# Performance work log

Measured on AMD Instinct MI355X. Metric: run time of the kernel, lower is better.

Reference implementation:

```python
import jax, jax.numpy as jnp
import numpy as np

N, E, B = 100000, 1200000, 512
IN_DIM, HID, K, NCLS = 64, 64, 3, 10


def setup_inputs() -> dict:
    key = jax.random.key(0)
    ks = jax.random.split(key, 10)
    features = jax.random.normal(ks[0], (N, IN_DIM), jnp.float32)
    edge_src = jax.random.randint(ks[1], (E,), 0, N)
    edge_dst = jax.random.randint(ks[2], (E,), 0, N)
    graph_ids = jnp.sort(jax.random.randint(ks[3], (N,), 0, B))
    s1 = float(1.0 / np.sqrt(IN_DIM))
    W1 = jax.random.uniform(ks[4], (IN_DIM, HID), jnp.float32, -s1, s1)
    b1 = jnp.zeros((HID,), jnp.float32)
    s2 = float(1.0 / np.sqrt(HID))
    W2 = jax.random.uniform(ks[5], (HID, HID), jnp.float32, -s2, s2)
    b2 = jnp.zeros((HID,), jnp.float32)
    s3 = float(1.0 / np.sqrt(HID * 3))
    cw = jax.random.uniform(ks[6], (HID, HID, 3), jnp.float32, -s3, s3)
    cb = jax.random.uniform(ks[7], (HID,), jnp.float32, -s3, s3)
    Wc = jax.random.uniform(ks[8], (HID, NCLS), jnp.float32, -s2, s2)
    bc = jax.random.uniform(ks[9], (NCLS,), jnp.float32, -s2, s2)
    return dict(features=features, edge_src=edge_src, edge_dst=edge_dst,
                graph_ids=graph_ids, num_graphs=B,
                W1=W1, b1=b1, W2=W2, b2=b2, cw=cw, cb=cb, Wc=Wc, bc=bc)


def graph_conv(h, src, dst, W, b, n_nodes):
    # DGL GraphConv, norm='both', allow_zero_in_degree (degrees clamped to 1)
    ones = jnp.ones((src.shape[0],), h.dtype)
    out_deg = jnp.zeros((n_nodes,), h.dtype).at[src].add(ones)
    in_deg = jnp.zeros((n_nodes,), h.dtype).at[dst].add(ones)
    norm_s = jax.lax.rsqrt(jnp.clip(out_deg, 1.0, None))
    norm_d = jax.lax.rsqrt(jnp.clip(in_deg, 1.0, None))
    m = (h * norm_s[:, None]) @ W  # weight first; math identical to agg-first
    agg = jnp.zeros((n_nodes, W.shape[1]), h.dtype).at[dst].add(m[src])
    return agg * norm_d[:, None] + b


def sort_pool(h, gid, num_graphs, k):
    # DGL SortPooling: sort each node's features ascending along feature dim,
    # then take top-k nodes per graph by last feature value (descending),
    # zero-padding graphs with < k nodes. Output [num_graphs, k*D].
    hs = jnp.sort(h, axis=-1)
    key = hs[:, -1]
    order = jnp.lexsort((-key, gid))  # gid asc, key desc
    gid_s = gid[order]
    hs_s = hs[order]
    n = gid.shape[0]
    start = jnp.full((num_graphs,), n).at[gid_s].min(jnp.arange(n))
    rank = jnp.arange(n) - start[gid_s]  # within-graph rank by key desc
    mask = rank < k
    slot = gid_s * k + jnp.clip(rank, 0, k - 1)
    out = jnp.zeros((num_graphs * k, hs.shape[-1]), h.dtype).at[slot].add(
        jnp.where(mask[:, None], hs_s, jnp.zeros((), h.dtype)))
    return out.reshape(num_graphs, k * hs.shape[-1])


def reference(features, edge_src, edge_dst, graph_ids, num_graphs,
              W1, b1, W2, b2, cw, cb, Wc, bc):
    n = features.shape[0]
    h = jax.nn.relu(graph_conv(features, edge_src, edge_dst, W1, b1, n))
    h = jax.nn.relu(graph_conv(h, edge_src, edge_dst, W2, b2, n))
    p = sort_pool(h, graph_ids, num_graphs, K)          # [B, K*HID]
    x = p.reshape(num_graphs, HID, K)                    # faithful torch reshape
    # Conv1d(kernel=3, stride=1) on length-3 input -> length-1 output
    y = jax.nn.relu(jnp.einsum('bct,oct->bo', x, cw) + cb)
    return y @ Wc + bc
```

## Files before the change

kernel.cpp:

```cpp
#include <hip/hip_runtime.h>
#include <hip/hip_bf16.h>


#define PART_F 25088
#define QUART_F (PART_F / 4)
#define MCH  128
#define MCHS 32

__device__ __forceinline__ unsigned long long nib2b(unsigned int x) {
  unsigned long long lo = x & 0x0F0F0F0Fu;
  unsigned long long hi = (x >> 4) & 0x0F0F0F0Fu;
  lo = (lo | (lo << 16)) & 0x0000FFFF0000FFFFull;
  lo = (lo | (lo << 8))  & 0x00FF00FF00FF00FFull;
  hi = (hi | (hi << 16)) & 0x0000FFFF0000FFFFull;
  hi = (hi | (hi << 8))  & 0x00FF00FF00FF00FFull;
  return lo | (hi << 8);
}

__global__ void __launch_bounds__(256) k_histgemm(
    const int* __restrict__ esrc, const int* __restrict__ edst,
    unsigned char* __restrict__ hd4, unsigned char* __restrict__ hs4,
    const float* __restrict__ in, const float* __restrict__ W,
    float* __restrict__ mout, int N, int E, int NP, int histBlocks) {
  __shared__ float smem[12800];
  const int t = threadIdx.x;
  if (blockIdx.x < histBlocks) {
    unsigned int* lc = (unsigned int*)smem;
    const int b = blockIdx.x;
    const int a = (b < MCH) ? 0 : 1;
    const int m = a ? (b - MCH) : b;
    const int mch = a ? MCHS : MCH;
    const int* __restrict__ arr = a ? esrc : edst;
    unsigned char* __restrict__ outp = a ? hs4 : hd4;
    const int nq = NP >> 5;
    {
      uint4 z = make_uint4(0u, 0u, 0u, 0u);
      uint4* lc16 = (uint4*)lc;
      for (int i = t; i < nq; i += 256) lc16[i] = z;
    }
    __syncthreads();
    const long long cb = (long long)m * E / mch;
    const long long ce = (long long)(m + 1) * E / mch;
    const long long a0 = min((cb + 3) & ~3LL, ce);
    const long long nv = (ce - a0) >> 2;
    for (long long e = cb + t; e < a0; e += 256) {
      int d = arr[e];
      atomicAdd(&lc[d >> 3], 1u << ((d & 7) * 4));
    }
    const int4* __restrict__ a4p = (const int4*)(arr + a0);
    for (long long i = t; i < nv; i += 256) {
      int4 v4 = a4p[i];
      atomicAdd(&lc[v4.x >> 3], 1u << ((v4.x & 7) * 4));
      atomicAdd(&lc[v4.y >> 3], 1u << ((v4.y & 7) * 4));
      atomicAdd(&lc[v4.z >> 3], 1u << ((v4.z & 7) * 4));
      atomicAdd(&lc[v4.w >> 3], 1u << ((v4.w & 7) * 4));
    }
    for (long long e = a0 + (nv << 2) + t; e < ce; e += 256) {
      int d = arr[e];
      atomicAdd(&lc[d >> 3], 1u << ((d & 7) * 4));
    }
    __syncthreads();
    uint4* slice16 = (uint4*)(outp + (size_t)m * (NP >> 1));
    const uint4* lc16 = (const uint4*)lc;
    for (int i = t; i < nq; i += 256) slice16[i] = lc16[i];
  } else {
    float* Wl = smem;
    float* Ac = smem + 4096;
    const int ch = (t & 7) * 8;
    const int nb = (t >> 3) * 4;
    for (int i = t; i < 1024; i += 256)
      ((float4*)Wl)[i] = ((const float4*)W)[i];
    const int gb = blockIdx.x - histBlocks;
    const int ng = gridDim.x - histBlocks;
    const int NT = (N + 127) >> 7;
    for (int tile = gb; tile < NT; tile += ng) {
      const int vbase = tile << 7;
      __syncthreads();
      for (int i = t; i < 2048; i += 256) {
        const int r = i >> 4;
        const int c = (i & 15) * 4;
        const int v = vbase + r;
        float4 val = make_float4(0.f, 0.f, 0.f, 0.f);
        if (v < N) val = *(const float4*)(in + (size_t)v * 64 + c);
        Ac[(c + 0) * 136 + r] = val.x;
        Ac[(c + 1) * 136 + r] = val.y;
        Ac[(c + 2) * 136 + r] = val.z;
        Ac[(c + 3) * 136 + r] = val.w;
      }
      __syncthreads();
      float acc[4][8];
#pragma unroll
      for (int j = 0; j < 4; ++j)
#pragma unroll
        for (int c = 0; c < 8; ++c) acc[j][c] = 0.f;
      for (int k = 0; k < 64; k += 4) {
#pragma unroll
        for (int kk = 0; kk < 4; ++kk) {
          const float4 aa = *(const float4*)&Ac[(k + kk) * 136 + nb];
          const float4 w0 = *(const float4*)&Wl[(k + kk) * 64 + ch];
          const float4 w1 = *(const float4*)&Wl[(k + kk) * 64 + ch + 4];
          const float an[4] = {aa.x, aa.y, aa.z, aa.w};
          const float wn[8] = {w0.x, w0.y, w0.z, w0.w, w1.x, w1.y, w1.z, w1.w};
#pragma unroll
          for (int j = 0; j < 4; ++j)
#pragma unroll
            for (int c = 0; c < 8; ++c)
              acc[j][c] = fmaf(an[j], wn[c], acc[j][c]);
        }
      }
#pragma unroll
      for (int j = 0; j < 4; ++j) {
        const int v = vbase + nb + j;
        if (v < N) {
          float4 o0, o1;
          o0.x = acc[j][0]; o0.y = acc[j][1]; o0.z = acc[j][2]; o0.w = acc[j][3];
          o1.x = acc[j][4]; o1.y = acc[j][5]; o1.z = acc[j][6]; o1.w = acc[j][7];
          *(float4*)(mout + (size_t)v * 64 + ch)     = o0;
          *(float4*)(mout + (size_t)v * 64 + ch + 4) = o1;
        }
      }
    }
  }
}

__global__ void __launch_bounds__(256) k_offscan(
    const unsigned char* __restrict__ hd4, const unsigned char* __restrict__ hs4,
    unsigned char* __restrict__ hd8,
    int* __restrict__ deg_d, float* __restrict__ norm_s, float* __restrict__ norm_d,
    int* __restrict__ gstart, int* __restrict__ rowptr, int* __restrict__ bsum,
    int B, int N, int NP) {
  __shared__ unsigned long long part[32][8];
  __shared__ unsigned long long spart[32][8];
  __shared__ int sums[256];
  const int t = threadIdx.x;
  const int s = t >> 3;
  const int c = t & 7;
  const int nb0 = blockIdx.x * 256;
  const int v0 = nb0 + s * 8;
  const int vt = nb0 + t;
  if (vt < B) gstart[vt] = 0x7f7f7f7f;
  const size_t half = (size_t)(NP >> 1);
  const unsigned char* __restrict__ hdp = hd4 + (v0 >> 1);
  const unsigned char* __restrict__ hsp = hs4 + (v0 >> 1);
  const int m0 = c * 16;
  const int m0s = c * 4;
  unsigned long long vals[16];
  unsigned long long tsum = 0ull, hsum = 0ull;
#pragma unroll
  for (int k = 0; k < 16; ++k) {
    unsigned int x = *(const unsigned int*)(hdp + (size_t)(m0 + k) * half);
    vals[k] = nib2b(x);
    tsum += vals[k];
  }
#pragma unroll
  for (int k = 0; k < 4; ++k) {
    unsigned int x = *(const unsigned int*)(hsp + (size_t)(m0s + k) * half);
    hsum += nib2b(x);
  }
  part[s][c] = tsum;
  spart[s][c] = hsum;
  __syncthreads();
  {
    unsigned long long run = 0ull;
#pragma unroll
    for (int cc = 0; cc < 8; ++cc)
      if (cc < c) run += part[s][cc];
#pragma unroll
    for (int k = 0; k < 16; ++k) {
      *(unsigned long long*)(hd8 + (size_t)(m0 + k) * NP + v0) = run;
      run += vals[k];
    }
  }
  unsigned long long dt = 0ull, ht = 0ull;
#pragma unroll
  for (int cc = 0; cc < 8; ++cc) {
    dt += part[t >> 3][cc];
    ht += spart[t >> 3][cc];
  }
  int dg = 0;
  if (vt < N) {
    dg = (int)((dt >> (8 * (t & 7))) & 0xffull);
    const int so = (int)((ht >> (8 * (t & 7))) & 0xffull);
    deg_d[vt] = dg;
    norm_d[vt] = rsqrtf((float)max(dg, 1));
    norm_s[vt] = rsqrtf((float)max(so, 1));
  }
  sums[t] = dg;
  __syncthreads();
  for (int off = 1; off < 256; off <<= 1) {
    int x = (t >= off) ? sums[t - off] : 0;
    __syncthreads();
    sums[t] += x;
    __syncthreads();
  }
  if (vt < N) rowptr[vt] = sums[t] - dg;
  if (t == 255) bsum[blockIdx.x] = sums[255];
}

__global__ void k_scan2(int* __restrict__ bsum, int nb) {
  __shared__ int sh[512];
  const int t = threadIdx.x;
  const int v = (t < nb) ? bsum[t] : 0;
  sh[t] = v;
  __syncthreads();
  for (int off = 1; off < 512; off <<= 1) {
    int x = (t >= off) ? sh[t - off] : 0;
    __syncthreads();
    sh[t] += x;
    __syncthreads();
  }
  if (t < nb) bsum[t] = sh[t] - v;
}

__global__ void k_fill2(const int* __restrict__ esrc, const int* __restrict__ edst,
                        const unsigned char* __restrict__ hd8, const int* __restrict__ rowptr,
                        const int* __restrict__ bsum, int* __restrict__ csr,
                        int N, int E, int PF, int NP) {
  __shared__ unsigned int cur4[QUART_F];
  const int b = blockIdx.x;
  const int p = b % PF;
  const int m = b / PF;
  const int base = p * PART_F;
  const int lim = min(PART_F, N - base);
  const unsigned char* slice = hd8 + (size_t)m * NP + (size_t)p * PART_F;
  const unsigned int* slice4 = (const unsigned int*)slice;
  for (int i = threadIdx.x; i < QUART_F; i += blockDim.x) cur4[i] = slice4[i];
  __syncthreads();
  const int* __restrict__ rp = rowptr + base;
  const long long cb = (long long)m * E / MCH;
  const long long ce = (long long)(m + 1) * E / MCH;
  const long long a0 = min((cb + 3) & ~3LL, ce);
  const long long nv = (ce - a0) >> 2;
  for (long long e = cb + threadIdx.x; e < a0; e += blockDim.x) {
    int d = edst[e] - base;
    if ((unsigned)d < (unsigned)lim) {
      unsigned int old = atomicAdd(&cur4[d >> 2], 1u << ((d & 3) * 8));
      csr[rp[d] + bsum[(base + d) >> 8] + ((old >> ((d & 3) * 8)) & 0xff)] = esrc[e];
    }
  }
  const int4* __restrict__ d4p = (const int4*)(edst + a0);
  const int4* __restrict__ s4p = (const int4*)(esrc + a0);
  for (long long i = threadIdx.x; i < nv; i += blockDim.x) {
    int4 d4 = d4p[i];
    int4 s4 = s4p[i];
    int d;
    d = d4.x - base;
    if ((unsigned)d < (unsigned)lim) {
      unsigned int old = atomicAdd(&cur4[d >> 2], 1u << ((d & 3) * 8));
      csr[rp[d] + bsum[(base + d) >> 8] + ((old >> ((d & 3) * 8)) & 0xff)] = s4.x;
    }
    d = d4.y - base;
    if ((unsigned)d < (unsigned)lim) {
      unsigned int old = atomicAdd(&cur4[d >> 2], 1u << ((d & 3) * 8));
      csr[rp[d] + bsum[(base + d) >> 8] + ((old >> ((d & 3) * 8)) & 0xff)] = s4.y;
    }
    d = d4.z - base;
    if ((unsigned)d < (unsigned)lim) {
      unsigned int old = atomicAdd(&cur4[d >> 2], 1u << ((d & 3) * 8));
      csr[rp[d] + bsum[(base + d) >> 8] + ((old >> ((d & 3) * 8)) & 0xff)] = s4.z;
    }
    d = d4.w - base;
    if ((unsigned)d < (unsigned)lim) {
      unsigned int old = atomicAdd(&cur4[d >> 2], 1u << ((d & 3) * 8));
      csr[rp[d] + bsum[(base + d) >> 8] + ((old >> ((d & 3) * 8)) & 0xff)] = s4.w;
    }
  }
  for (long long e = a0 + (nv << 2) + threadIdx.x; e < ce; e += blockDim.x) {
    int d = edst[e] - base;
    if ((unsigned)d < (unsigned)lim) {
      unsigned int old = atomicAdd(&cur4[d >> 2], 1u << ((d & 3) * 8));
      csr[rp[d] + bsum[(base + d) >> 8] + ((old >> ((d & 3) * 8)) & 0xff)] = esrc[e];
    }
  }
}

__global__ void __launch_bounds__(256) k_gemm64(
    const float* __restrict__ in, const float* __restrict__ norm,
    const float* __restrict__ W, float* __restrict__ out, int N) {
  __shared__ float Wl[4096];
  __shared__ float Ac[64 * 136];
  const int t = threadIdx.x;
  const int ch = (t & 7) * 8;
  const int nb = (t >> 3) * 4;
  for (int i = t; i < 1024; i += 256)
    ((float4*)Wl)[i] = ((const float4*)W)[i];
  const int NT = (N + 127) >> 7;
  for (int tile = blockIdx.x; tile < NT; tile += gridDim.x) {
    const int vbase = tile << 7;
    __syncthreads();
    for (int i = t; i < 2048; i += 256) {
      const int r = i >> 4;
      const int c = (i & 15) * 4;
      const int v = vbase + r;
      float4 val = make_float4(0.f, 0.f, 0.f, 0.f);
      if (v < N) val = *(const float4*)(in + (size_t)v * 64 + c);
      Ac[(c + 0) * 136 + r] = val.x;
      Ac[(c + 1) * 136 + r] = val.y;
      Ac[(c + 2) * 136 + r] = val.z;
      Ac[(c + 3) * 136 + r] = val.w;
    }
    __syncthreads();
    float acc[4][8];
#pragma unroll
    for (int j = 0; j < 4; ++j)
#pragma unroll
      for (int c = 0; c < 8; ++c) acc[j][c] = 0.f;
    for (int k = 0; k < 64; k += 4) {
#pragma unroll
      for (int kk = 0; kk < 4; ++kk) {
        const float4 aa = *(const float4*)&Ac[(k + kk) * 136 + nb];
        const float4 w0 = *(const float4*)&Wl[(k + kk) * 64 + ch];
        const float4 w1 = *(const float4*)&Wl[(k + kk) * 64 + ch + 4];
        const float an[4] = {aa.x, aa.y, aa.z, aa.w};
        const float wn[8] = {w0.x, w0.y, w0.z, w0.w, w1.x, w1.y, w1.z, w1.w};
#pragma unroll
        for (int j = 0; j < 4; ++j)
#pragma unroll
          for (int c = 0; c < 8; ++c)
            acc[j][c] = fmaf(an[j], wn[c], acc[j][c]);
      }
    }
#pragma unroll
    for (int j = 0; j < 4; ++j) {
      const int v = vbase + nb + j;
      if (v < N) {
        const float nm = norm[v];
        float4 o0, o1;
        o0.x = acc[j][0] * nm; o0.y = acc[j][1] * nm;
        o0.z = acc[j][2] * nm; o0.w = acc[j][3] * nm;
        o1.x = acc[j][4] * nm; o1.y = acc[j][5] * nm;
        o1.z = acc[j][6] * nm; o1.w = acc[j][7] * nm;
        *(float4*)(out + (size_t)v * 64 + ch)     = o0;
        *(float4*)(out + (size_t)v * 64 + ch + 4) = o1;
      }
    }
  }
}

__global__ void k_gather(const float* __restrict__ m, const int* __restrict__ rowptr,
                         const int* __restrict__ bsum,
                         const int* __restrict__ deg, const float* __restrict__ norm_d,
                         const float* __restrict__ bias, const int* __restrict__ csr,
                         const float* __restrict__ nsrc,
                         const int* __restrict__ gid, int* __restrict__ gstart,
                         float* __restrict__ h, float* __restrict__ key, int N) {
  const int wpb = blockDim.x >> 6;
  const int nwaves = gridDim.x * wpb;
  const int lane = threadIdx.x & 63;
  const int chb = (lane & 7) * 8;
  const int grp = lane >> 3;
  const float4 b0 = *(const float4*)(bias + chb);
  const float4 b1 = *(const float4*)(bias + chb + 4);
  for (int w = blockIdx.x * wpb + (threadIdx.x >> 6); w < N; w += nwaves) {
    if (gid != nullptr && lane == 0) {
      int g = gid[w];
      if (w == 0 || gid[w - 1] != g) gstart[g] = w;
    }
    const int start = rowptr[w] + bsum[w >> 8];
    const int cnt = deg[w];
    float4 a00 = make_float4(0.f, 0.f, 0.f, 0.f);
    float4 a01 = make_float4(0.f, 0.f, 0.f, 0.f);
    float4 a10 = make_float4(0.f, 0.f, 0.f, 0.f);
    float4 a11 = make_float4(0.f, 0.f, 0.f, 0.f);
    int i = grp;
    if (nsrc != nullptr) {
      for (; i + 8 < cnt; i += 16) {
        int s0 = csr[start + i];
        int s1 = csr[start + i + 8];
        float n0 = nsrc[s0], n1 = nsrc[s1];
        const float* r0 = m + (size_t)s0 * 64 + chb;
        const float* r1 = m + (size_t)s1 * 64 + chb;
        const float4 v00 = *(const float4*)r0;
        const float4 v01 = *(const float4*)(r0 + 4);
        const float4 v10 = *(const float4*)r1;
        const float4 v11 = *(const float4*)(r1 + 4);
        a00.x = fmaf(v00.x, n0, a00.x); a00.y = fmaf(v00.y, n0, a00.y);
        a00.z = fmaf(v00.z, n0, a00.z); a00.w = fmaf(v00.w, n0, a00.w);
        a01.x = fmaf(v01.x, n0, a01.x); a01.y = fmaf(v01.y, n0, a01.y);
        a01.z = fmaf(v01.z, n0, a01.z); a01.w = fmaf(v01.w, n0, a01.w);
        a10.x = fmaf(v10.x, n1, a10.x); a10.y = fmaf(v10.y, n1, a10.y);
        a10.z = fmaf(v10.z, n1, a10.z); a10.w = fmaf(v10.w, n1, a10.w);
        a11.x = fmaf(v11.x, n1, a11.x); a11.y = fmaf(v11.y, n1, a11.y);
        a11.z = fmaf(v11.z, n1, a11.z); a11.w = fmaf(v11.w, n1, a11.w);
      }
      if (i < cnt) {
        int s0 = csr[start + i];
        float n0 = nsrc[s0];
        const float* r0 = m + (size_t)s0 * 64 + chb;
        const float4 v00 = *(const float4*)r0;
        const float4 v01 = *(const float4*)(r0 + 4);
        a00.x = fmaf(v00.x, n0, a00.x); a00.y = fmaf(v00.y, n0, a00.y);
        a00.z = fmaf(v00.z, n0, a00.z); a00.w = fmaf(v00.w, n0, a00.w);
        a01.x = fmaf(v01.x, n0, a01.x); a01.y = fmaf(v01.y, n0, a01.y);
        a01.z = fmaf(v01.z, n0, a01.z); a01.w = fmaf(v01.w, n0, a01.w);
      }
    } else {
      for (; i + 8 < cnt; i += 16) {
        int s0 = csr[start + i];
        int s1 = csr[start + i + 8];
        const float* r0 = m + (size_t)s0 * 64 + chb;
        const float* r1 = m + (size_t)s1 * 64 + chb;
        const float4 v00 = *(const float4*)r0;
        const float4 v01 = *(const float4*)(r0 + 4);
        const float4 v10 = *(const float4*)r1;
        const float4 v11 = *(const float4*)(r1 + 4);
        a00.x += v00.x; a00.y += v00.y; a00.z += v00.z; a00.w += v00.w;
        a01.x += v01.x; a01.y += v01.y; a01.z += v01.z; a01.w += v01.w;
        a10.x += v10.x; a10.y += v10.y; a10.z += v10.z; a10.w += v10.w;
        a11.x += v11.x; a11.y += v11.y; a11.z += v11.z; a11.w += v11.w;
      }
      if (i < cnt) {
        int s0 = csr[start + i];
        const float* r0 = m + (size_t)s0 * 64 + chb;
        const float4 v00 = *(const float4*)r0;
        const float4 v01 = *(const float4*)(r0 + 4);
        a00.x += v00.x; a00.y += v00.y; a00.z += v00.z; a00.w += v00.w;
        a01.x += v01.x; a01.y += v01.y; a01.z += v01.z; a01.w += v01.w;
      }
    }
    a00.x += a10.x; a00.y += a10.y; a00.z += a10.z; a00.w += a10.w;
    a01.x += a11.x; a01.y += a11.y; a01.z += a11.z; a01.w += a11.w;
#pragma unroll
    for (int off = 8; off <= 32; off <<= 1) {
      a00.x += __shfl_xor(a00.x, off, 64);
      a00.y += __shfl_xor(a00.y, off, 64);
      a00.z += __shfl_xor(a00.z, off, 64);
      a00.w += __shfl_xor(a00.w, off, 64);
      a01.x += __shfl_xor(a01.x, off, 64);
      a01.y += __shfl_xor(a01.y, off, 64);
      a01.z += __shfl_xor(a01.z, off, 64);
      a01.w += __shfl_xor(a01.w, off, 64);
    }
    const float nd = norm_d[w];
    float4 o0, o1;
    o0.x = fmaxf(fmaf(a00.x, nd, b0.x), 0.f);
    o0.y = fmaxf(fmaf(a00.y, nd, b0.y), 0.f);
    o0.z = fmaxf(fmaf(a00.z, nd, b0.z), 0.f);
    o0.w = fmaxf(fmaf(a00.w, nd, b0.w), 0.f);
    o1.x = fmaxf(fmaf(a01.x, nd, b1.x), 0.f);
    o1.y = fmaxf(fmaf(a01.y, nd, b1.y), 0.f);
    o1.z = fmaxf(fmaf(a01.z, nd, b1.z), 0.f);
    o1.w = fmaxf(fmaf(a01.w, nd, b1.w), 0.f);
    if (h != nullptr && grp == 0) {
      *(float4*)(h + (size_t)w * 64 + chb)     = o0;
      *(float4*)(h + (size_t)w * 64 + chb + 4) = o1;
    }
    if (key != nullptr) {
      float mx = fmaxf(fmaxf(fmaxf(o0.x, o0.y), fmaxf(o0.z, o0.w)),
                       fmaxf(fmaxf(o1.x, o1.y), fmaxf(o1.z, o1.w)));
#pragma unroll
      for (int off = 1; off < 8; off <<= 1) mx = fmaxf(mx, __shfl_xor(mx, off, 64));
      if (lane == 0) key[w] = mx;
    }
  }
}

__global__ void __launch_bounds__(256) k_tail(
    const float* __restrict__ key, const int* __restrict__ gstart,
    const float* __restrict__ m, const int* __restrict__ rowptr,
    const int* __restrict__ bsum, const int* __restrict__ deg,
    const float* __restrict__ norm_d, const float* __restrict__ bias,
    const int* __restrict__ csr,
    const float* __restrict__ cw, const float* __restrict__ cb,
    const float* __restrict__ Wc, const float* __restrict__ bc,
    float* __restrict__ out, int B, int N) {
  __shared__ int sel[3];
  __shared__ float prow[192];
  const int b = blockIdx.x;
  const int wid = threadIdx.x >> 6;
  const int lane = threadIdx.x & 63;

  if (wid == 0) {
    const int gs = gstart[b];
    int g2 = b + 1;
    while (g2 < B && gstart[g2] >= N) ++g2;
    const int ns = (g2 < B) ? gstart[g2] : N;
    const int s = gs;
    const int c = (gs < N) ? (ns - gs) : 0;
    float v0 = -1.f, v1 = -1.f, v2 = -1.f;
    int i0 = 0x7fffffff, i1 = 0x7fffffff, i2 = 0x7fffffff;
    for (int i = s + lane; i < s + c; i += 64) {
      float kv = key[i];
      if (kv > v0 || (kv == v0 && i < i0)) {
        v2 = v1; i2 = i1; v1 = v0; i1 = i0; v0 = kv; i0 = i;
      } else if (kv > v1 || (kv == v1 && i < i1)) {
        v2 = v1; i2 = i1; v1 = kv; i1 = i;
      } else if (kv > v2 || (kv == v2 && i < i2)) {
        v2 = kv; i2 = i;
      }
    }
    int ptr = 0;
    for (int r = 0; r < 3; ++r) {
      float mv = (ptr == 0) ? v0 : (ptr == 1) ? v1 : (ptr == 2) ? v2 : -1.f;
      int   mi = (ptr == 0) ? i0 : (ptr == 1) ? i1 : (ptr == 2) ? i2 : 0x7fffffff;
      float bv = mv; int bi = mi;
#pragma unroll
      for (int off = 32; off; off >>= 1) {
        float ov = __shfl_xor(bv, off, 64);
        int   oi = __shfl_xor(bi, off, 64);
        if (ov > bv || (ov == bv && oi < bi)) { bv = ov; bi = oi; }
      }
      if (bi == mi && ptr < 3) ptr++;
      if (lane == 0) sel[r] = (bi == 0x7fffffff) ? -1 : bi;
    }
  }
  __syncthreads();
  if (wid < 3) {
    const int node = sel[wid];
    if (node >= 0) {
      const int chb = (lane & 7) * 8;
      const int grp = lane >> 3;
      const int start = rowptr[node] + bsum[node >> 8];
      const int cnt = deg[node];
      float4 a00 = make_float4(0.f, 0.f, 0.f, 0.f);
      float4 a01 = make_float4(0.f, 0.f, 0.f, 0.f);
      float4 a10 = make_float4(0.f, 0.f, 0.f, 0.f);
      float4 a11 = make_float4(0.f, 0.f, 0.f, 0.f);
      int i = grp;
      for (; i + 8 < cnt; i += 16) {
        int s0 = csr[start + i];
        int s1 = csr[start + i + 8];
        const float* r0 = m + (size_t)s0 * 64 + chb;
        const float* r1 = m + (size_t)s1 * 64 + chb;
        const float4 v00 = *(const float4*)r0;
        const float4 v01 = *(const float4*)(r0 + 4);
        const float4 v10 = *(const float4*)r1;
        const float4 v11 = *(const float4*)(r1 + 4);
        a00.x += v00.x; a00.y += v00.y; a00.z += v00.z; a00.w += v00.w;
        a01.x += v01.x; a01.y += v01.y; a01.z += v01.z; a01.w += v01.w;
        a10.x += v10.x; a10.y += v10.y; a10.z += v10.z; a10.w += v10.w;
        a11.x += v11.x; a11.y += v11.y; a11.z += v11.z; a11.w += v11.w;
      }
      if (i < cnt) {
        int s0 = csr[start + i];
        const float* r0 = m + (size_t)s0 * 64 + chb;
        const float4 v00 = *(const float4*)r0;
        const float4 v01 = *(const float4*)(r0 + 4);
        a00.x += v00.x; a00.y += v00.y; a00.z += v00.z; a00.w += v00.w;
        a01.x += v01.x; a01.y += v01.y; a01.z += v01.z; a01.w += v01.w;
      }
      a00.x += a10.x; a00.y += a10.y; a00.z += a10.z; a00.w += a10.w;
      a01.x += a11.x; a01.y += a11.y; a01.z += a11.z; a01.w += a11.w;
#pragma unroll
      for (int off = 8; off <= 32; off <<= 1) {
        a00.x += __shfl_xor(a00.x, off, 64);
        a00.y += __shfl_xor(a00.y, off, 64);
        a00.z += __shfl_xor(a00.z, off, 64);
        a00.w += __shfl_xor(a00.w, off, 64);
        a01.x += __shfl_xor(a01.x, off, 64);
        a01.y += __shfl_xor(a01.y, off, 64);
        a01.z += __shfl_xor(a01.z, off, 64);
        a01.w += __shfl_xor(a01.w, off, 64);
      }
      const float nd = norm_d[node];
      const float4 b0 = *(const float4*)(bias + chb);
      const float4 b1 = *(const float4*)(bias + chb + 4);
      float4 o0, o1;
      o0.x = fmaxf(fmaf(a00.x, nd, b0.x), 0.f);
      o0.y = fmaxf(fmaf(a00.y, nd, b0.y), 0.f);
      o0.z = fmaxf(fmaf(a00.z, nd, b0.z), 0.f);
      o0.w = fmaxf(fmaf(a00.w, nd, b0.w), 0.f);
      o1.x = fmaxf(fmaf(a01.x, nd, b1.x), 0.f);
      o1.y = fmaxf(fmaf(a01.y, nd, b1.y), 0.f);
      o1.z = fmaxf(fmaf(a01.z, nd, b1.z), 0.f);
      o1.w = fmaxf(fmaf(a01.w, nd, b1.w), 0.f);
      if (grp == 0) {
        *(float4*)&prow[wid * 64 + chb]     = o0;
        *(float4*)&prow[wid * 64 + chb + 4] = o1;
      }
    } else {
      prow[wid * 64 + lane] = 0.f;
    }
  }
  __syncthreads();
  if (wid < 3) {
    float v = prow[wid * 64 + lane];
    if (sel[wid] >= 0) {
      for (int k2 = 2; k2 <= 64; k2 <<= 1) {
        for (int j = k2 >> 1; j > 0; j >>= 1) {
          float o = __shfl_xor(v, j, 64);
          bool up = ((lane & k2) == 0);
          bool lower = ((lane & j) == 0);
          v = (lower == up) ? fminf(v, o) : fmaxf(v, o);
        }
      }
    }
    prow[wid * 64 + lane] = v;
  }
  __syncthreads();
  if (wid == 0) {
    float y = cb[lane];
    for (int j = 0; j < 192; ++j) y = fmaf(prow[j], cw[lane * 192 + j], y);
    float ry = fmaxf(y, 0.f);
    for (int c = 0; c < 10; ++c) {
      float s = ry * Wc[lane * 10 + c];
#pragma unroll
      for (int off = 32; off; off >>= 1) s += __shfl_xor(s, off, 64);
      if (lane == 0) out[b * 10 + c] = s + bc[c];
    }
  }
}

extern "C" void kernel_launch(void* const* d_in, const int* in_sizes, int n_in,
                              void* d_out, int out_size, void* d_ws, size_t ws_size,
                              hipStream_t stream) {
  const float* features = (const float*)d_in[0];
  const int*   esrc     = (const int*)d_in[1];
  const int*   edst     = (const int*)d_in[2];
  const int*   gid      = (const int*)d_in[3];
  const float* W1 = (const float*)d_in[5];
  const float* b1 = (const float*)d_in[6];
  const float* W2 = (const float*)d_in[7];
  const float* b2 = (const float*)d_in[8];
  const float* cw = (const float*)d_in[9];
  const float* cb = (const float*)d_in[10];
  const float* Wc = (const float*)d_in[11];
  const float* bc = (const float*)d_in[12];
  float* out = (float*)d_out;

  const int N = in_sizes[0] / 64;
  const int E = in_sizes[1];
  const int B = out_size / 10;
  const size_t N64 = (size_t)N * 64;
  const int nscan = (N + 255) / 256;
  const int PF = (N + PART_F - 1) / PART_F;
  const int NP = PF * PART_F;
  const int NT = (N + 127) / 128;
  const int histBlocks = MCH + MCHS;

  float* bufA   = (float*)d_ws;
  float* bufB   = bufA + N64;
  int*   deg_d  = (int*)(bufB + N64);
  float* norm_s = (float*)(deg_d + N);
  float* norm_d = norm_s + N;
  float* key    = norm_d + N;
  int*   rowptr = (int*)(key + N);
  int*   csr    = rowptr + N;
  int*   bsum   = csr + E;
  int*   gstart = bsum + 512;
  unsigned char* hd4 = (unsigned char*)(((size_t)(gstart + B) + 15) & ~(size_t)15);
  unsigned char* hs4 = hd4 + (size_t)MCH  * (NP >> 1);
  unsigned char* hd8 = hs4 + (size_t)MCHS * (NP >> 1);

  const int TB = 256;

  k_histgemm<<<histBlocks + NT, TB, 0, stream>>>(esrc, edst, hd4, hs4,
                                                 features, W1, bufA,
                                                 N, E, NP, histBlocks);
  k_offscan<<<nscan, 256, 0, stream>>>(hd4, hs4, hd8, deg_d, norm_s, norm_d,
                                       gstart, rowptr, bsum, B, N, NP);
  k_scan2<<<1, 512, 0, stream>>>(bsum, nscan);
  k_fill2<<<PF * MCH, TB, 0, stream>>>(esrc, edst, hd8, rowptr, bsum, csr,
                                       N, E, PF, NP);

  const int GB = 2048;

  k_gather<<<GB, TB, 0, stream>>>(bufA, rowptr, bsum, deg_d, norm_d, b1,
                                  csr, norm_s, nullptr, nullptr,
                                  bufB, nullptr, N);

  k_gemm64<<<NT, TB, 0, stream>>>(bufB, norm_s, W2, bufA, N);
  k_gather<<<GB, TB, 0, stream>>>(bufA, rowptr, bsum, deg_d, norm_d, b2,
                                  csr, nullptr, gid, gstart,
                                  nullptr, key, N);

  k_tail<<<B, TB, 0, stream>>>(key, gstart, bufA, rowptr, bsum, deg_d,
                               norm_d, b2, csr, cw, cb, Wc, bc, out, B, N);
}
```

Measured before the change: 296.8 us.

## Replace nibble-packed LDS histograms with global atomics for degree and CSR build

Measured after the change: 412.7 us. 1.39x slower.

```diff
diff --git a/kernel.cpp b/kernel.cpp
--- a/kernel.cpp
+++ b/kernel.cpp
@@ -2,67 +2,31 @@
 #include <hip/hip_bf16.h>
 
 
-#define PART_F 25088
-#define QUART_F (PART_F / 4)
-#define MCH  128
-#define MCHS 32
-
-__device__ __forceinline__ unsigned long long nib2b(unsigned int x) {
-  unsigned long long lo = x & 0x0F0F0F0Fu;
-  unsigned long long hi = (x >> 4) & 0x0F0F0F0Fu;
-  lo = (lo | (lo << 16)) & 0x0000FFFF0000FFFFull;
-  lo = (lo | (lo << 8))  & 0x00FF00FF00FF00FFull;
-  hi = (hi | (hi << 16)) & 0x0000FFFF0000FFFFull;
-  hi = (hi | (hi << 8))  & 0x00FF00FF00FF00FFull;
-  return lo | (hi << 8);
-}
-
-__global__ void __launch_bounds__(256) k_histgemm(
+__global__ void __launch_bounds__(256) k_deggemm(
     const int* __restrict__ esrc, const int* __restrict__ edst,
-    unsigned char* __restrict__ hd4, unsigned char* __restrict__ hs4,
+    int* __restrict__ deg_d, int* __restrict__ sdeg,
     const float* __restrict__ in, const float* __restrict__ W,
-    float* __restrict__ mout, int N, int E, int NP, int histBlocks) {
+    float* __restrict__ mout, int N, int E, int degBlocks) {
   __shared__ float smem[12800];
   const int t = threadIdx.x;
-  if (blockIdx.x < histBlocks) {
-    unsigned int* lc = (unsigned int*)smem;
-    const int b = blockIdx.x;
-    const int a = (b < MCH) ? 0 : 1;
-    const int m = a ? (b - MCH) : b;
-    const int mch = a ? MCHS : MCH;
-    const int* __restrict__ arr = a ? esrc : edst;
-    unsigned char* __restrict__ outp = a ? hs4 : hd4;
-    const int nq = NP >> 5;
-    {
-      uint4 z = make_uint4(0u, 0u, 0u, 0u);
-      uint4* lc16 = (uint4*)lc;
-      for (int i = t; i < nq; i += 256) lc16[i] = z;
-    }
-    __syncthreads();
-    const long long cb = (long long)m * E / mch;
-    const long long ce = (long long)(m + 1) * E / mch;
-    const long long a0 = min((cb + 3) & ~3LL, ce);
-    const long long nv = (ce - a0) >> 2;
-    for (long long e = cb + t; e < a0; e += 256) {
-      int d = arr[e];
-      atomicAdd(&lc[d >> 3], 1u << ((d & 7) * 4));
-    }
-    const int4* __restrict__ a4p = (const int4*)(arr + a0);
-    for (long long i = t; i < nv; i += 256) {
-      int4 v4 = a4p[i];
-      atomicAdd(&lc[v4.x >> 3], 1u << ((v4.x & 7) * 4));
-      atomicAdd(&lc[v4.y >> 3], 1u << ((v4.y & 7) * 4));
-      atomicAdd(&lc[v4.z >> 3], 1u << ((v4.z & 7) * 4));
-      atomicAdd(&lc[v4.w >> 3], 1u << ((v4.w & 7) * 4));
-    }
-    for (long long e = a0 + (nv << 2) + t; e < ce; e += 256) {
-      int d = arr[e];
-      atomicAdd(&lc[d >> 3], 1u << ((d & 7) * 4));
-    }
-    __syncthreads();
-    uint4* slice16 = (uint4*)(outp + (size_t)m * (NP >> 1));
-    const uint4* lc16 = (const uint4*)lc;
-    for (int i = t; i < nq; i += 256) slice16[i] = lc16[i];
+  if (blockIdx.x < degBlocks) {
+    const long long e4 = (long long)E >> 2;
+    const long long stride = (long long)degBlocks * 256;
+    const int4* __restrict__ s4 = (const int4*)esrc;
+    const int4* __restrict__ d4 = (const int4*)edst;
+    for (long long i = (long long)blockIdx.x * 256 + t; i < e4; i += stride) {
+      int4 d = d4[i];
+      atomicAdd(&deg_d[d.x], 1); atomicAdd(&deg_d[d.y], 1);
+      atomicAdd(&deg_d[d.z], 1); atomicAdd(&deg_d[d.w], 1);
+      int4 s = s4[i];
+      atomicAdd(&sdeg[s.x], 1); atomicAdd(&sdeg[s.y], 1);
+      atomicAdd(&sdeg[s.z], 1); atomicAdd(&sdeg[s.w], 1);
+    }
+    for (long long e = (e4 << 2) + (long long)blockIdx.x * 256 + t; e < E;
+         e += stride) {
+      atomicAdd(&deg_d[edst[e]], 1);
+      atomicAdd(&sdeg[esrc[e]], 1);
+    }
   } else {
     float* Wl = smem;
     float* Ac = smem + 4096;
@@ -70,8 +34,8 @@
     const int nb = (t >> 3) * 4;
     for (int i = t; i < 1024; i += 256)
       ((float4*)Wl)[i] = ((const float4*)W)[i];
-    const int gb = blockIdx.x - histBlocks;
-    const int ng = gridDim.x - histBlocks;
+    const int gb = blockIdx.x - degBlocks;
+    const int ng = gridDim.x - degBlocks;
     const int NT = (N + 127) >> 7;
     for (int tile = gb; tile < NT; tile += ng) {
       const int vbase = tile << 7;
@@ -123,67 +87,20 @@
   }
 }
 
-__global__ void __launch_bounds__(256) k_offscan(
-    const unsigned char* __restrict__ hd4, const unsigned char* __restrict__ hs4,
-    unsigned char* __restrict__ hd8,
-    int* __restrict__ deg_d, float* __restrict__ norm_s, float* __restrict__ norm_d,
-    int* __restrict__ gstart, int* __restrict__ rowptr, int* __restrict__ bsum,
-    int B, int N, int NP) {
-  __shared__ unsigned long long part[32][8];
-  __shared__ unsigned long long spart[32][8];
+__global__ void __launch_bounds__(256) k_scan1(
+    const int* __restrict__ deg, const int* __restrict__ sdeg,
+    float* __restrict__ norm_s, float* __restrict__ norm_d,
+    int* __restrict__ cur, int* __restrict__ rowptr, int* __restrict__ bsum,
+    int N) {
   __shared__ int sums[256];
   const int t = threadIdx.x;
-  const int s = t >> 3;
-  const int c = t & 7;
-  const int nb0 = blockIdx.x * 256;
-  const int v0 = nb0 + s * 8;
-  const int vt = nb0 + t;
-  if (vt < B) gstart[vt] = 0x7f7f7f7f;
-  const size_t half = (size_t)(NP >> 1);
-  const unsigned char* __restrict__ hdp = hd4 + (v0 >> 1);
-  const unsigned char* __restrict__ hsp = hs4 + (v0 >> 1);
-  const int m0 = c * 16;
-  const int m0s = c * 4;
-  unsigned long long vals[16];
-  unsigned long long tsum = 0ull, hsum = 0ull;
-#pragma unroll
-  for (int k = 0; k < 16; ++k) {
-    unsigned int x = *(const unsigned int*)(hdp + (size_t)(m0 + k) * half);
-    vals[k] = nib2b(x);
-    tsum += vals[k];
-  }
-#pragma unroll
-  for (int k = 0; k < 4; ++k) {
-    unsigned int x = *(const unsigned int*)(hsp + (size_t)(m0s + k) * half);
-    hsum += nib2b(x);
-  }
-  part[s][c] = tsum;
-  spart[s][c] = hsum;
-  __syncthreads();
-  {
-    unsigned long long run = 0ull;
-#pragma unroll
-    for (int cc = 0; cc < 8; ++cc)
-      if (cc < c) run += part[s][cc];
-#pragma unroll
-    for (int k = 0; k < 16; ++k) {
-      *(unsigned long long*)(hd8 + (size_t)(m0 + k) * NP + v0) = run;
-      run += vals[k];
-    }
-  }
-  unsigned long long dt = 0ull, ht = 0ull;
-#pragma unroll
-  for (int cc = 0; cc < 8; ++cc) {
-    dt += part[t >> 3][cc];
-    ht += spart[t >> 3][cc];
-  }
+  const int v = blockIdx.x * 256 + t;
   int dg = 0;
-  if (vt < N) {
-    dg = (int)((dt >> (8 * (t & 7))) & 0xffull);
-    const int so = (int)((ht >> (8 * (t & 7))) & 0xffull);
-    deg_d[vt] = dg;
-    norm_d[vt] = rsqrtf((float)max(dg, 1));
-    norm_s[vt] = rsqrtf((float)max(so, 1));
+  if (v < N) {
+    dg = deg[v];
+    norm_d[v] = rsqrtf((float)max(dg, 1));
+    norm_s[v] = rsqrtf((float)max(sdeg[v], 1));
+    cur[v] = 0;
   }
   sums[t] = dg;
   __syncthreads();
@@ -193,7 +110,7 @@
     sums[t] += x;
     __syncthreads();
   }
-  if (vt < N) rowptr[vt] = sums[t] - dg;
+  if (v < N) rowptr[v] = sums[t] - dg;
   if (t == 255) bsum[blockIdx.x] = sums[255];
 }
 
@@ -212,65 +129,33 @@
   if (t < nb) bsum[t] = sh[t] - v;
 }
 
-__global__ void k_fill2(const int* __restrict__ esrc, const int* __restrict__ edst,
-                        const unsigned char* __restrict__ hd8, const int* __restrict__ rowptr,
-                        const int* __restrict__ bsum, int* __restrict__ csr,
-                        int N, int E, int PF, int NP) {
-  __shared__ unsigned int cur4[QUART_F];
-  const int b = blockIdx.x;
-  const int p = b % PF;
-  const int m = b / PF;
-  const int base = p * PART_F;
-  const int lim = min(PART_F, N - base);
-  const unsigned char* slice = hd8 + (size_t)m * NP + (size_t)p * PART_F;
-  const unsigned int* slice4 = (const unsigned int*)slice;
-  for (int i = threadIdx.x; i < QUART_F; i += blockDim.x) cur4[i] = slice4[i];
-  __syncthreads();
-  const int* __restrict__ rp = rowptr + base;
-  const long long cb = (long long)m * E / MCH;
-  const long long ce = (long long)(m + 1) * E / MCH;
-  const long long a0 = min((cb + 3) & ~3LL, ce);
-  const long long nv = (ce - a0) >> 2;
-  for (long long e = cb + threadIdx.x; e < a0; e += blockDim.x) {
-    int d = edst[e] - base;
-    if ((unsigned)d < (unsigned)lim) {
-      unsigned int old = atomicAdd(&cur4[d >> 2], 1u << ((d & 3) * 8));
-      csr[rp[d] + bsum[(base + d) >> 8] + ((old >> ((d & 3) * 8)) & 0xff)] = esrc[e];
-    }
-  }
-  const int4* __restrict__ d4p = (const int4*)(edst + a0);
-  const int4* __restrict__ s4p = (const int4*)(esrc + a0);
-  for (long long i = threadIdx.x; i < nv; i += blockDim.x) {
-    int4 d4 = d4p[i];
-    int4 s4 = s4p[i];
-    int d;
-    d = d4.x - base;
-    if ((unsigned)d < (unsigned)lim) {
-      unsigned int old = atomicAdd(&cur4[d >> 2], 1u << ((d & 3) * 8));
-      csr[rp[d] + bsum[(base + d) >> 8] + ((old >> ((d & 3) * 8)) & 0xff)] = s4.x;
-    }
-    d = d4.y - base;
-    if ((unsigned)d < (unsigned)lim) {
-      unsigned int old = atomicAdd(&cur4[d >> 2], 1u << ((d & 3) * 8));
-      csr[rp[d] + bsum[(base + d) >> 8] + ((old >> ((d & 3) * 8)) & 0xff)] = s4.y;
-    }
-    d = d4.z - base;
-    if ((unsigned)d < (unsigned)lim) {
-      unsigned int old = atomicAdd(&cur4[d >> 2], 1u << ((d & 3) * 8));
-      csr[rp[d] + bsum[(base + d) >> 8] + ((old >> ((d & 3) * 8)) & 0xff)] = s4.z;
-    }
-    d = d4.w - base;
-    if ((unsigned)d < (unsigned)lim) {
-      unsigned int old = atomicAdd(&cur4[d >> 2], 1u << ((d & 3) * 8));
-      csr[rp[d] + bsum[(base + d) >> 8] + ((old >> ((d & 3) * 8)) & 0xff)] = s4.w;
-    }
-  }
-  for (long long e = a0 + (nv << 2) + threadIdx.x; e < ce; e += blockDim.x) {
-    int d = edst[e] - base;
-    if ((unsigned)d < (unsigned)lim) {
-      unsigned int old = atomicAdd(&cur4[d >> 2], 1u << ((d & 3) * 8));
-      csr[rp[d] + bsum[(base + d) >> 8] + ((old >> ((d & 3) * 8)) & 0xff)] = esrc[e];
-    }
+__global__ void __launch_bounds__(256) k_fill(
+    const int* __restrict__ esrc, const int* __restrict__ edst,
+    const int* __restrict__ rowptr, const int* __restrict__ bsum,
+    int* __restrict__ cur, int* __restrict__ csr, int E) {
+  const long long e4 = (long long)E >> 2;
+  const long long stride = (long long)gridDim.x * 256;
+  const int4* __restrict__ s4 = (const int4*)esrc;
+  const int4* __restrict__ d4 = (const int4*)edst;
+  for (long long i = (long long)blockIdx.x * 256 + threadIdx.x; i < e4;
+       i += stride) {
+    int4 d = d4[i];
+    int4 s = s4[i];
+    int slot;
+    slot = atomicAdd(&cur[d.x], 1);
+    csr[rowptr[d.x] + bsum[d.x >> 8] + slot] = s.x;
+    slot = atomicAdd(&cur[d.y], 1);
+    csr[rowptr[d.y] + bsum[d.y >> 8] + slot] = s.y;
+    slot = atomicAdd(&cur[d.z], 1);
+    csr[rowptr[d.z] + bsum[d.z >> 8] + slot] = s.z;
+    slot = atomicAdd(&cur[d.w], 1);
+    csr[rowptr[d.w] + bsum[d.w >> 8] + slot] = s.w;
+  }
+  for (long long e = (e4 << 2) + (long long)blockIdx.x * 256 + threadIdx.x;
+       e < E; e += stride) {
+    int d = edst[e];
+    int slot = atomicAdd(&cur[d], 1);
+    csr[rowptr[d] + bsum[d >> 8] + slot] = esrc[e];
   }
 }
 
@@ -623,35 +508,35 @@
   const int B = out_size / 10;
   const size_t N64 = (size_t)N * 64;
   const int nscan = (N + 255) / 256;
-  const int PF = (N + PART_F - 1) / PART_F;
-  const int NP = PF * PART_F;
   const int NT = (N + 127) / 128;
-  const int histBlocks = MCH + MCHS;
+  const int degBlocks = 512;
 
   float* bufA   = (float*)d_ws;
   float* bufB   = bufA + N64;
   int*   deg_d  = (int*)(bufB + N64);
-  float* norm_s = (float*)(deg_d + N);
+  int*   sdeg   = deg_d + N;
+  float* norm_s = (float*)(sdeg + N);
   float* norm_d = norm_s + N;
   float* key    = norm_d + N;
   int*   rowptr = (int*)(key + N);
-  int*   csr    = rowptr + N;
+  int*   cur    = rowptr + N;
+  int*   csr    = cur + N;
   int*   bsum   = csr + E;
   int*   gstart = bsum + 512;
-  unsigned char* hd4 = (unsigned char*)(((size_t)(gstart + B) + 15) & ~(size_t)15);
-  unsigned char* hs4 = hd4 + (size_t)MCH  * (NP >> 1);
-  unsigned char* hd8 = hs4 + (size_t)MCHS * (NP >> 1);
 
   const int TB = 256;
 
-  k_histgemm<<<histBlocks + NT, TB, 0, stream>>>(esrc, edst, hd4, hs4,
-                                                 features, W1, bufA,
-                                                 N, E, NP, histBlocks);
-  k_offscan<<<nscan, 256, 0, stream>>>(hd4, hs4, hd8, deg_d, norm_s, norm_d,
-                                       gstart, rowptr, bsum, B, N, NP);
+  hipMemsetAsync(deg_d, 0, (size_t)N * 4, stream);
+  hipMemsetAsync(sdeg, 0, (size_t)N * 4, stream);
+  hipMemsetAsync(gstart, 0x7f, (size_t)B * 4, stream);
+
+  k_deggemm<<<degBlocks + NT, TB, 0, stream>>>(esrc, edst, deg_d, sdeg,
+                                               features, W1, bufA,
+                                               N, E, degBlocks);
+  k_scan1<<<nscan, TB, 0, stream>>>(deg_d, sdeg, norm_s, norm_d, cur,
+                                    rowptr, bsum, N);
   k_scan2<<<1, 512, 0, stream>>>(bsum, nscan);
-  k_fill2<<<PF * MCH, TB, 0, stream>>>(esrc, edst, hd8, rowptr, bsum, csr,
-                                       N, E, PF, NP);
+  k_fill<<<1024, TB, 0, stream>>>(esrc, edst, rowptr, bsum, cur, csr, E);
 
   const int GB = 2048;
 
```
